# Kernel optimization log

Measured on AMD Instinct MI355X. Metric: run time of the kernel, lower is better.

## Reference

```python
import jax, jax.numpy as jnp
import numpy as np

B, S, H, DH = 8, 2048, 4, 32
D = H * DH  # all_head_size = true_hidden_size = 128


def setup_inputs() -> dict:
    key = jax.random.key(0)
    ks = jax.random.split(key, 9)
    inp = {
        "query_tensor": jax.random.normal(ks[0], (B, S, D), dtype=jnp.float32),
        "key_tensor": jax.random.normal(ks[1], (B, S, D), dtype=jnp.float32),
        "value_tensor": jax.random.normal(ks[2], (B, S, D), dtype=jnp.float32),
        "attention_mask": jnp.zeros((B, 1, 1, S), dtype=jnp.float32),
        "head_mask": jnp.ones((1, H, 1, 1), dtype=jnp.float32),
        "Wq": jax.random.normal(ks[3], (D, D), dtype=jnp.float32) * 0.02,
        "bq": jnp.zeros((D,), dtype=jnp.float32),
        "Wk": jax.random.normal(ks[4], (D, D), dtype=jnp.float32) * 0.02,
        "bk": jnp.zeros((D,), dtype=jnp.float32),
        "Wv": jax.random.normal(ks[5], (D, D), dtype=jnp.float32) * 0.02,
        "bv": jnp.zeros((D,), dtype=jnp.float32),
    }
    return inp


def _split_heads(x):
    # (B, S, D) -> (B, H, S, DH)
    return x.reshape(B, S, H, DH).transpose(0, 2, 1, 3)


def reference(query_tensor, key_tensor, value_tensor, attention_mask, head_mask,
              Wq, bq, Wk, bk, Wv, bv):
    q = _split_heads(query_tensor @ Wq + bq)   # (B,H,S,DH)
    k = _split_heads(key_tensor @ Wk + bk)
    v = _split_heads(value_tensor @ Wv + bv)

    scale = 1.0 / jnp.sqrt(jnp.float32(DH))
    scores = jnp.einsum("bhqd,bhkd->bhqk", q, k) * scale + attention_mask
    probs = jax.nn.softmax(scores, axis=-1)
    # dropout is identity at inference (training=False)
    probs = probs * head_mask
    ctx = jnp.einsum("bhqk,bhkd->bhqd", probs, v)  # (B,H,S,DH)
    ctx = ctx.transpose(0, 2, 1, 3).reshape(B, S, D)
    return ctx
```

## Files before the change

kernel.cpp:

```cpp
#include <hip/hip_runtime.h>
#include <hip/hip_bf16.h>
#include <math.h>

#define B_ 8
#define S_ 2048
#define H_ 4
#define DH_ 32
#define D_ 128
#define BS_ (B_ * S_)
#define LOG2E 1.4426950408889634f
#define QSCALE (0.17677669529663687f * LOG2E)

typedef float f32x4  __attribute__((ext_vector_type(4)));
typedef float f32x16 __attribute__((ext_vector_type(16)));
typedef short s16x8  __attribute__((ext_vector_type(8)));

__device__ __forceinline__ unsigned short bf(float x) {
    return __builtin_bit_cast(unsigned short, __float2bfloat16(x));
}
__device__ __forceinline__ float bf2f(unsigned short u) {
    return __builtin_bit_cast(float, (unsigned int)u << 16);
}
__device__ __forceinline__ unsigned int pk2(float a, float b) {
    unsigned int r;
    asm("v_cvt_pk_bf16_f32 %0, %1, %2" : "=v"(r) : "v"(a), "v"(b));
    return r;
}
__device__ __forceinline__ void pswap(unsigned int& a, unsigned int& b) {
    asm volatile("v_permlane32_swap_b32 %0, %1" : "+v"(a), "+v"(b));
}

#define OFF_Q  0u
#define OFF_K  2097152u
#define OFF_V  4194304u
#define OFF_W  6291456u
#define OFF_E  6389760u

__global__ __launch_bounds__(256) void wprep(
    const float* __restrict__ Wq, const float* __restrict__ Wk, const float* __restrict__ Wv,
    const float* __restrict__ maskg,
    unsigned short* __restrict__ Wt, unsigned short* __restrict__ Em)
{
    if (blockIdx.z == 3) {
        const int id16 = blockIdx.y * 4 + blockIdx.x;
        const int base = id16 * 1024 + threadIdx.x * 4;
        float4 m4 = *(const float4*)&maskg[base];
        ushort4 o;
        o.x = bf(__builtin_amdgcn_exp2f(m4.x * LOG2E));
        o.y = bf(__builtin_amdgcn_exp2f(m4.y * LOG2E));
        o.z = bf(__builtin_amdgcn_exp2f(m4.z * LOG2E));
        o.w = bf(__builtin_amdgcn_exp2f(m4.w * LOG2E));
        *(ushort4*)&Em[base] = o;
        return;
    }
    const float* W = (blockIdx.z == 0) ? Wq : (blockIdx.z == 1) ? Wk : Wv;
    unsigned short* Oh = Wt + (size_t)blockIdx.z * D_ * D_;
    unsigned short* Ol = Oh + 3 * D_ * D_;
    __shared__ float tf[32][36];
    const int t = threadIdx.x;
    const int kt = blockIdx.x * 32, ct = blockIdx.y * 32;
    {
        int kl = t >> 3, cl = (t & 7) * 4;
        float4 w4 = *(const float4*)&W[(size_t)(kt + kl) * D_ + ct + cl];
        tf[kl][cl + 0] = w4.x; tf[kl][cl + 1] = w4.y;
        tf[kl][cl + 2] = w4.z; tf[kl][cl + 3] = w4.w;
    }
    __syncthreads();
    {
        int cl = t >> 3, kl = (t & 7) * 4;
        ushort4 oh, ol;
        float v;
        v = tf[kl + 0][cl]; oh.x = bf(v); ol.x = bf(v - bf2f(oh.x));
        v = tf[kl + 1][cl]; oh.y = bf(v); ol.y = bf(v - bf2f(oh.y));
        v = tf[kl + 2][cl]; oh.z = bf(v); ol.z = bf(v - bf2f(oh.z));
        v = tf[kl + 3][cl]; oh.w = bf(v); ol.w = bf(v - bf2f(oh.w));
        *(ushort4*)&Oh[(size_t)(ct + cl) * D_ + kt + kl] = oh;
        *(ushort4*)&Ol[(size_t)(ct + cl) * D_ + kt + kl] = ol;
    }
}

__global__ __launch_bounds__(256) void qkv_mfma(
    const float* __restrict__ Xq, const float* __restrict__ Xk, const float* __restrict__ Xv,
    const unsigned short* __restrict__ Wt, const float* __restrict__ maskg,
    const float* __restrict__ bq, const float* __restrict__ bk, const float* __restrict__ bv,
    unsigned short* __restrict__ Qo, unsigned short* __restrict__ Kf,
    unsigned short* __restrict__ Vf)
{
    const int mode = blockIdx.z, chalf = blockIdx.y;
    const float* X; const float* bias; float scl;
    if (mode == 0)      { X = Xq; bias = bq; scl = QSCALE; }
    else if (mode == 1) { X = Xk; bias = bk; scl = 1.f; }
    else                { X = Xv; bias = bv; scl = 1.f; }
    const unsigned short* WmH = Wt + (size_t)mode * D_ * D_;
    const unsigned short* WmL = WmH + 3 * D_ * D_;

    __shared__ __align__(16) unsigned short xa[2 * 32 * 136];
    __shared__ __align__(16) unsigned short wt[2 * 64 * 136];

    const int t = threadIdx.x;
    const long row0 = (long)blockIdx.x * 32;

    #pragma unroll
    for (int j = 0; j < 8; j++) {
        int idx = t + 256 * j;
        int part = idx >> 10, i2 = idx & 1023;
        int r = i2 >> 4, c16 = i2 & 15;
        const unsigned short* src = part ? WmL : WmH;
        uint4 v = *(const uint4*)&src[(size_t)(chalf * 64 + r) * D_ + c16 * 8];
        *(uint4*)&wt[part * 8704 + r * 136 + c16 * 8] = v;
    }
    #pragma unroll
    for (int j = 0; j < 4; j++) {
        int idx = t + 256 * j;
        int r = idx >> 5, c4 = idx & 31;
        float4 v = *(const float4*)(X + (row0 + r) * D_ + c4 * 4);
        ushort4 ph, pl;
        ph.x = bf(v.x); pl.x = bf(v.x - bf2f(ph.x));
        ph.y = bf(v.y); pl.y = bf(v.y - bf2f(ph.y));
        ph.z = bf(v.z); pl.z = bf(v.z - bf2f(ph.z));
        ph.w = bf(v.w); pl.w = bf(v.w - bf2f(ph.w));
        *(ushort4*)&xa[r * 136 + c4 * 4] = ph;
        *(ushort4*)&xa[4352 + r * 136 + c4 * 4] = pl;
    }
    __syncthreads();

    const int w = t >> 6, lane = t & 63, lo = lane & 15, hi = lane >> 4;
    const int mf = w >> 1, nb = (w & 1) * 2;
    f32x4 acc[2] = {};
    #pragma unroll
    for (int kk = 0; kk < 4; kk++) {
        const int ko = kk * 32 + hi * 8;
        s16x8 ah = *(const s16x8*)&xa[(mf * 16 + lo) * 136 + ko];
        s16x8 al = *(const s16x8*)&xa[4352 + (mf * 16 + lo) * 136 + ko];
        #pragma unroll
        for (int n2 = 0; n2 < 2; n2++) {
            const int nf = nb + n2;
            s16x8 bh2 = *(const s16x8*)&wt[(nf * 16 + lo) * 136 + ko];
            s16x8 bl2 = *(const s16x8*)&wt[8704 + (nf * 16 + lo) * 136 + ko];
            acc[n2] = __builtin_amdgcn_mfma_f32_16x16x32_bf16(ah, bh2, acc[n2], 0, 0, 0);
            acc[n2] = __builtin_amdgcn_mfma_f32_16x16x32_bf16(al, bh2, acc[n2], 0, 0, 0);
            acc[n2] = __builtin_amdgcn_mfma_f32_16x16x32_bf16(ah, bl2, acc[n2], 0, 0, 0);
        }
    }
    __syncthreads();

    const long b_i = row0 >> 11;
    const long s0g = row0 & 2047;

    if (mode < 2) {
        #pragma unroll
        for (int n2 = 0; n2 < 2; n2++) {
            int c_l = (nb + n2) * 16 + lo;
            float bb = bias[chalf * 64 + c_l];
            #pragma unroll
            for (int r = 0; r < 4; r++) {
                int s = mf * 16 + hi * 4 + r;
                xa[s * 72 + c_l] = bf((acc[n2][r] + bb) * scl);
            }
        }
        __syncthreads();
        int s = t >> 3, part = t & 7;
        int c_g = chalf * 64 + part * 8;
        int h = c_g >> 5, dd = c_g & 31;
        long s_i = s0g + s;
        int bh = (int)(b_i * H_ + h);
        uint4 val = *(const uint4*)&xa[s * 72 + part * 8];
        if (mode == 0) {
            *(uint4*)(Qo + ((size_t)bh * S_ + s_i) * DH_ + dd) = val;
        } else {
            int fr = dd >> 4, hwd = (dd >> 3) & 1;
            size_t off = ((((size_t)bh * 64 + (s_i >> 5)) * 2 + fr) * 64
                          + (s_i & 31) + hwd * 32) * 8;
            *(uint4*)(Kf + off) = val;
        }
    } else {
        float emr[4];
        #pragma unroll
        for (int r = 0; r < 4; r++) {
            const int s_l = mf * 16 + hi * 4 + r;
            emr[r] = __builtin_amdgcn_exp2f(maskg[b_i * S_ + s0g + s_l] * LOG2E);
        }
        #pragma unroll
        for (int n2 = 0; n2 < 2; n2++) {
            int c_l = (nb + n2) * 16 + lo;
            float bb = bias[chalf * 64 + c_l];
            #pragma unroll
            for (int r = 0; r < 4; r++) {
                int s = mf * 16 + hi * 4 + r;
                xa[c_l * 68 + s] = bf((acc[n2][r] + bb) * emr[r]);
            }
        }
        __syncthreads();
        if (t < 128) {
            int c_l = t >> 1, sh2 = (t & 1) * 16;
            int c_g = chalf * 64 + c_l;
            int h = c_g >> 5, dd = c_g & 31;
            long key0 = s0g + sh2;
            int bh = (int)(b_i * H_ + h);
            size_t base = (((size_t)bh * 128 + (key0 >> 4)) * 64 + dd) * 8;
            uint2 p0 = *(const uint2*)&xa[c_l * 68 + sh2 + 0];
            uint2 p1 = *(const uint2*)&xa[c_l * 68 + sh2 + 4];
            uint2 p2 = *(const uint2*)&xa[c_l * 68 + sh2 + 8];
            uint2 p3 = *(const uint2*)&xa[c_l * 68 + sh2 + 12];
            *(uint4*)(Vf + base)       = make_uint4(p0.x, p0.y, p1.x, p1.y);
            *(uint4*)(Vf + base + 256) = make_uint4(p2.x, p2.y, p3.x, p3.y);
        }
    }
}

__global__ __launch_bounds__(512, 2) void flash_mfma(
    const unsigned short* __restrict__ Qg, const unsigned short* __restrict__ Kfg,
    const unsigned short* __restrict__ Vfg, const unsigned short* __restrict__ Emg,
    const float* __restrict__ head_mask, float* __restrict__ Out)
{
    __shared__ float ms[2][2][64][33];

    const int t = threadIdx.x, w = t >> 6, lane = t & 63;
    const int l31 = lane & 31, hw = lane >> 5;
    const int kq = w & 3, qh = w >> 2;

    const int lid = blockIdx.x;
    const int xcd = lid & 7, ser = lid >> 3;
    const int bh = xcd * 4 + (ser >> 5);
    const int qi = ser & 31;
    const int b = bh >> 2, h = bh & 3;
    const int q0 = qi * 64 + qh * 32;

    const unsigned short* qp = Qg + ((size_t)bh * S_ + q0 + l31) * DH_ + hw * 8;
    const s16x8 qf0 = *(const s16x8*)qp;
    const s16x8 qf1 = *(const s16x8*)(qp + 16);

    const unsigned short* kp = Kfg + (size_t)bh * 65536 + (size_t)kq * 1024 + (size_t)lane * 8;
    const unsigned short* vp = Vfg + (size_t)bh * 65536 + (size_t)kq * 1024 + (size_t)lane * 8;
    const unsigned short* ep = Emg + (size_t)b * S_ + kq * 32 + hw * 8;

    s16x8 kf0 = *(const s16x8*)kp;
    s16x8 kf1 = *(const s16x8*)(kp + 512);
    s16x8 vf0 = *(const s16x8*)vp;
    s16x8 vf1 = *(const s16x8*)(vp + 512);
    s16x8 ef0 = *(const s16x8*)(ep);
    s16x8 ef1 = *(const s16x8*)(ep + 16);

    f32x16 ctx = {}, lacc = {};
    const f32x16 z16 = {};

    for (int tile = 0; tile < 16; tile++) {
        s16x8 kn0, kn1, vn0, vn1, en0, en1;
        if (tile < 15) {
            const unsigned short* kp2 = kp + (size_t)(tile + 1) * 4096;
            const unsigned short* vp2 = vp + (size_t)(tile + 1) * 4096;
            const unsigned short* ep2 = ep + (size_t)(tile + 1) * 128;
            kn0 = *(const s16x8*)kp2;
            kn1 = *(const s16x8*)(kp2 + 512);
            vn0 = *(const s16x8*)vp2;
            vn1 = *(const s16x8*)(vp2 + 512);
            en0 = *(const s16x8*)ep2;
            en1 = *(const s16x8*)(ep2 + 16);
        }

        __builtin_amdgcn_s_setprio(1);
        f32x16 s = __builtin_amdgcn_mfma_f32_32x32x16_bf16(kf0, qf0, z16, 0, 0, 0);
        s = __builtin_amdgcn_mfma_f32_32x32x16_bf16(kf1, qf1, s, 0, 0, 0);
        __builtin_amdgcn_s_setprio(0);

        unsigned int pd[8];
        #pragma unroll
        for (int j = 0; j < 8; j++) {
            const float p0 = __builtin_amdgcn_exp2f(s[2 * j]);
            const float p1 = __builtin_amdgcn_exp2f(s[2 * j + 1]);
            pd[j] = pk2(p0, p1);
        }
        pswap(pd[0], pd[2]); pswap(pd[1], pd[3]);
        pswap(pd[4], pd[6]); pswap(pd[5], pd[7]);
        const s16x8 pa0 = __builtin_bit_cast(s16x8, make_uint4(pd[0], pd[1], pd[2], pd[3]));
        const s16x8 pa1 = __builtin_bit_cast(s16x8, make_uint4(pd[4], pd[5], pd[6], pd[7]));

        __builtin_amdgcn_s_setprio(1);
        ctx  = __builtin_amdgcn_mfma_f32_32x32x16_bf16(pa0, vf0, ctx, 0, 0, 0);
        lacc = __builtin_amdgcn_mfma_f32_32x32x16_bf16(pa0, ef0, lacc, 0, 0, 0);
        ctx  = __builtin_amdgcn_mfma_f32_32x32x16_bf16(pa1, vf1, ctx, 0, 0, 0);
        lacc = __builtin_amdgcn_mfma_f32_32x32x16_bf16(pa1, ef1, lacc, 0, 0, 0);
        __builtin_amdgcn_s_setprio(0);

        if (tile < 15) {
            kf0 = kn0; kf1 = kn1; vf0 = vn0; vf1 = vn1; ef0 = en0; ef1 = en1;
        }
    }

    if (kq >= 2) {
        float* d = &ms[qh][kq - 2][lane][0];
        #pragma unroll
        for (int r = 0; r < 16; r++) { d[r] = ctx[r]; d[16 + r] = lacc[r]; }
    }
    __syncthreads();
    if (kq < 2) {
        const float* sr = &ms[qh][kq][lane][0];
        #pragma unroll
        for (int r = 0; r < 16; r++) { ctx[r] += sr[r]; lacc[r] += sr[16 + r]; }
    }
    __syncthreads();
    if (kq == 1) {
        float* d = &ms[qh][0][lane][0];
        #pragma unroll
        for (int r = 0; r < 16; r++) { d[r] = ctx[r]; d[16 + r] = lacc[r]; }
    }
    __syncthreads();
    if (kq == 0) {
        const float* sr = &ms[qh][0][lane][0];
        #pragma unroll
        for (int r = 0; r < 16; r++) { ctx[r] += sr[r]; lacc[r] += sr[16 + r]; }
        const float hm = head_mask[h];
        #pragma unroll
        for (int r = 0; r < 16; r++) {
            const int qrow = (r & 3) + 8 * (r >> 2) + 4 * hw;
            Out[((size_t)b * S_ + q0 + qrow) * D_ + h * DH_ + l31] = ctx[r] * hm / lacc[r];
        }
    }
}

extern "C" void kernel_launch(void* const* d_in, const int* in_sizes, int n_in,
                              void* d_out, int out_size, void* d_ws, size_t ws_size,
                              hipStream_t stream) {
    const float* Xq   = (const float*)d_in[0];
    const float* Xk   = (const float*)d_in[1];
    const float* Xv   = (const float*)d_in[2];
    const float* mask = (const float*)d_in[3];
    const float* hm   = (const float*)d_in[4];
    const float* Wq   = (const float*)d_in[5];
    const float* bq   = (const float*)d_in[6];
    const float* Wk   = (const float*)d_in[7];
    const float* bk   = (const float*)d_in[8];
    const float* Wv   = (const float*)d_in[9];
    const float* bv   = (const float*)d_in[10];
    float* out = (float*)d_out;

    unsigned short* ws = (unsigned short*)d_ws;
    unsigned short* Qo = ws + OFF_Q;
    unsigned short* Kf = ws + OFF_K;
    unsigned short* Vf = ws + OFF_V;
    unsigned short* Wt = ws + OFF_W;
    unsigned short* Em = ws + OFF_E;

    wprep<<<dim3(4, 4, 4), 256, 0, stream>>>(Wq, Wk, Wv, mask, Wt, Em);
    qkv_mfma<<<dim3(BS_ / 32, 2, 3), 256, 0, stream>>>(Xq, Xk, Xv, Wt, mask,
                                                       bq, bk, bv, Qo, Kf, Vf);
    flash_mfma<<<dim3(1024), 512, 0, stream>>>(Qo, Kf, Vf, Em, hm, out);
}
```

Baseline: 56.16 us.

## Stage K/V tiles through double-buffered LDS via global_load_lds

Each tile's K and V are now loaded by all eight waves together with direct global-to-LDS loads into a double-buffered shared array, and each wave reads its fragments from LDS. Previously, waves that share a key quarter but serve different query halves each fetched the same K/V data from global memory into registers. The change halves redundant global/L2 traffic and frees prefetch registers. In exchange it adds a block-wide barrier per tile and extra LDS reads.

```diff
diff --git a/kernel.cpp b/kernel.cpp
--- a/kernel.cpp
+++ b/kernel.cpp
@@ -28,6 +28,11 @@
 }
 __device__ __forceinline__ void pswap(unsigned int& a, unsigned int& b) {
     asm volatile("v_permlane32_swap_b32 %0, %1" : "+v"(a), "+v"(b));
+}
+__device__ __forceinline__ void gll16(const void* g, void* l) {
+    __builtin_amdgcn_global_load_lds(
+        (const __attribute__((address_space(1))) unsigned int*)(g),
+        (__attribute__((address_space(3))) unsigned int*)(l), 16, 0, 0);
 }
 
 #define OFF_Q  0u
@@ -213,6 +218,8 @@
     const unsigned short* __restrict__ Vfg, const unsigned short* __restrict__ Emg,
     const float* __restrict__ head_mask, float* __restrict__ Out)
 {
+    __shared__ __align__(16) unsigned short ksh[2][4096];
+    __shared__ __align__(16) unsigned short vsh[2][4096];
     __shared__ float ms[2][2][64][33];
 
     const int t = threadIdx.x, w = t >> 6, lane = t & 63;
@@ -230,33 +237,37 @@
     const s16x8 qf0 = *(const s16x8*)qp;
     const s16x8 qf1 = *(const s16x8*)(qp + 16);
 
-    const unsigned short* kp = Kfg + (size_t)bh * 65536 + (size_t)kq * 1024 + (size_t)lane * 8;
-    const unsigned short* vp = Vfg + (size_t)bh * 65536 + (size_t)kq * 1024 + (size_t)lane * 8;
-    const unsigned short* ep = Emg + (size_t)b * S_ + kq * 32 + hw * 8;
-
-    s16x8 kf0 = *(const s16x8*)kp;
-    s16x8 kf1 = *(const s16x8*)(kp + 512);
-    s16x8 vf0 = *(const s16x8*)vp;
-    s16x8 vf1 = *(const s16x8*)(vp + 512);
+    const size_t kvbase = (size_t)bh * 65536;
+    const unsigned short* ksrc = Kfg + kvbase + (size_t)w * 512 + (size_t)lane * 8;
+    const unsigned short* vsrc = Vfg + kvbase + (size_t)w * 512 + (size_t)lane * 8;
+    const unsigned short* ep   = Emg + (size_t)b * S_ + kq * 32 + hw * 8;
+
+    gll16(ksrc, &ksh[0][w * 512]);
+    gll16(vsrc, &vsh[0][w * 512]);
     s16x8 ef0 = *(const s16x8*)(ep);
     s16x8 ef1 = *(const s16x8*)(ep + 16);
+    __syncthreads();
 
     f32x16 ctx = {}, lacc = {};
     const f32x16 z16 = {};
 
     for (int tile = 0; tile < 16; tile++) {
-        s16x8 kn0, kn1, vn0, vn1, en0, en1;
+        const int cur = tile & 1, nxt = cur ^ 1;
+
+        s16x8 en0, en1;
         if (tile < 15) {
-            const unsigned short* kp2 = kp + (size_t)(tile + 1) * 4096;
-            const unsigned short* vp2 = vp + (size_t)(tile + 1) * 4096;
-            const unsigned short* ep2 = ep + (size_t)(tile + 1) * 128;
-            kn0 = *(const s16x8*)kp2;
-            kn1 = *(const s16x8*)(kp2 + 512);
-            vn0 = *(const s16x8*)vp2;
-            vn1 = *(const s16x8*)(vp2 + 512);
-            en0 = *(const s16x8*)ep2;
-            en1 = *(const s16x8*)(ep2 + 16);
-        }
+            gll16(ksrc + (size_t)(tile + 1) * 4096, &ksh[nxt][w * 512]);
+            gll16(vsrc + (size_t)(tile + 1) * 4096, &vsh[nxt][w * 512]);
+            en0 = *(const s16x8*)(ep + (tile + 1) * 128);
+            en1 = *(const s16x8*)(ep + (tile + 1) * 128 + 16);
+        }
+
+        const unsigned short* kb = &ksh[cur][kq * 1024];
+        const unsigned short* vb = &vsh[cur][kq * 1024];
+        const s16x8 kf0 = *(const s16x8*)(kb + (size_t)lane * 8);
+        const s16x8 kf1 = *(const s16x8*)(kb + 512 + (size_t)lane * 8);
+        const s16x8 vf0 = *(const s16x8*)(vb + (size_t)lane * 8);
+        const s16x8 vf1 = *(const s16x8*)(vb + 512 + (size_t)lane * 8);
 
         __builtin_amdgcn_s_setprio(1);
         f32x16 s = __builtin_amdgcn_mfma_f32_32x32x16_bf16(kf0, qf0, z16, 0, 0, 0);
@@ -282,9 +293,8 @@
         lacc = __builtin_amdgcn_mfma_f32_32x32x16_bf16(pa1, ef1, lacc, 0, 0, 0);
         __builtin_amdgcn_s_setprio(0);
 
-        if (tile < 15) {
-            kf0 = kn0; kf1 = kn1; vf0 = vn0; vf1 = vn1; ef0 = en0; ef1 = en1;
-        }
+        __syncthreads();
+        if (tile < 15) { ef0 = en0; ef1 = en1; }
     }
 
     if (kq >= 2) {
```

New measurement: 61.02 us. 1.09x slower.
